# Kernel tuning notes

Measured on AMD Instinct MI355X. Metric: run time of the kernel, lower is better.

Reference implementation:

```python
import jax, jax.numpy as jnp
import numpy as np

N_NODES = 50000
N_EDGES = 800000
F_DIM = 128
K_RBF = 5
NUM_BLOCKS = 5
NUM_RES = 2  # residuals ModuleList is overwritten; only num_atom_residual layers exist
NUM_ELEM = 20
CUTOFF = 10.0
LOG2 = float(np.log(2.0))


def shifted_softplus(x):
    return jax.nn.softplus(x) - LOG2


def rbf_expand(D):
    # D: [E]; ExponentialRBF with cutoff=10, K=5.
    # softplus(softplus_inverse(x)) == x, so centers/widths are the raw values.
    centers = jnp.linspace(1.0, float(np.exp(-CUTOFF)), K_RBF)          # [K]
    width = jnp.float32((0.5 / ((1.0 - np.exp(-CUTOFF)) / K_RBF)) ** 2)  # scalar
    x = D / CUTOFF
    x3 = x ** 3; x4 = x3 * x; x5 = x4 * x
    cut = jnp.where(x < 1.0, 1.0 - 6.0 * x5 + 15.0 * x4 - 10.0 * x3, 0.0)  # [E]
    return cut[:, None] * jnp.exp(-width * (jnp.exp(-D)[:, None] - centers) ** 2)  # [E,K]


def residual(x, w1, b1, w2, b2):
    # ResidualLayer: x + dense2(dense1(act(x))) (dropout = identity in eval)
    y = shifted_softplus(x)
    return x + (y @ w1.T + b1) @ w2.T + b2


def setup_inputs() -> dict:
    key = jax.random.key(0)
    ks = jax.random.split(key, 20)
    s = 1.0 / np.sqrt(F_DIM)
    B, R = NUM_BLOCKS, NUM_RES
    inp = {
        'atom_types': jax.random.randint(ks[0], (N_NODES,), 0, NUM_ELEM),
        'edge_src': jax.random.randint(ks[1], (N_EDGES,), 0, N_NODES),
        'edge_dst': jax.random.randint(ks[2], (N_EDGES,), 0, N_NODES),
        'pos': jax.random.normal(ks[3], (N_NODES, 3), jnp.float32) * 3.0,
        'emb_table': jax.random.normal(ks[4], (NUM_ELEM, F_DIM), jnp.float32),
        'k2f_w': jax.random.normal(ks[5], (B, F_DIM, K_RBF), jnp.float32) * 0.4,
        'wi': jax.random.normal(ks[6], (B, F_DIM, F_DIM), jnp.float32) * s,
        'bi': jnp.zeros((B, F_DIM), jnp.float32),
        'wj': jax.random.normal(ks[7], (B, F_DIM, F_DIM), jnp.float32) * s,
        'bj': jnp.zeros((B, F_DIM), jnp.float32),
        'wd': jax.random.normal(ks[8], (B, F_DIM, F_DIM), jnp.float32) * s,
        'bd': jnp.zeros((B, F_DIM), jnp.float32),
        'u': jax.random.uniform(ks[9], (B, F_DIM), jnp.float32),
        'res_w1': jax.random.normal(ks[10], (B, R, F_DIM, F_DIM), jnp.float32) * s,
        'res_b1': jnp.zeros((B, R, F_DIM), jnp.float32),
        'res_w2': jax.random.normal(ks[11], (B, R, F_DIM, F_DIM), jnp.float32) * s,
        'res_b2': jnp.zeros((B, R, F_DIM), jnp.float32),
    }
    return inp


def reference(atom_types, edge_src, edge_dst, pos, emb_table,
              k2f_w, wi, bi, wj, bj, wd, bd, u,
              res_w1, res_b1, res_w2, res_b2):
    # edge distances and RBF features are geometry-only: compute once
    dist = jnp.linalg.norm(pos[edge_src] - pos[edge_dst], axis=-1)  # [E]
    rbf = rbf_expand(dist)                                          # [E,K]

    h = emb_table[atom_types]                                       # [N,F]
    for b in range(NUM_BLOCKS):
        x = shifted_softplus(h)  # pre-activation (dropout = identity)
        # dense_i / dense_j are linear -> apply on nodes, then gather per edge
        hi = x @ wi[b].T + bi[b]
        hj = x @ wj[b].T + bj[b]
        ai = hi[edge_dst]                                           # [E,F] target i
        g = rbf @ k2f_w[b].T                                        # [E,F]
        aj = g * hj[edge_src]                                       # [E,F]
        m = ai + aj
        for r in range(NUM_RES):
            m = residual(m, res_w1[b, r], res_b1[b, r], res_w2[b, r], res_b2[b, r])
        m = shifted_softplus(m)
        new = u[b] * ai + m @ wd[b].T + bd[b]
        for r in range(NUM_RES):  # same residual layers reused (as in source)
            new = residual(new, res_w1[b, r], res_b1[b, r], res_w2[b, r], res_b2[b, r])
        h = jax.ops.segment_sum(new, edge_dst, num_segments=N_NODES)  # aggr='add'
    return h
```

## Files before the change

### kernel.cpp

```cpp
#include <hip/hip_runtime.h>
#include <stdint.h>

#define FD 128
#define NNODES 50000
#define NEDGES 800000
#define EB 64

typedef __attribute__((ext_vector_type(8))) short v8s;
typedef __attribute__((ext_vector_type(4))) float v4f;

__device__ __forceinline__ unsigned short f2bf(float f) {
  union { float f; unsigned int u; } v; v.f = f;
  unsigned int r = v.u + 0x7fffu + ((v.u >> 16) & 1u);
  return (unsigned short)(r >> 16);
}
__device__ __forceinline__ float bf2f(unsigned short b) {
  union { unsigned int u; float f; } v; v.u = ((unsigned int)b) << 16;
  return v.f;
}
__device__ __forceinline__ float sspf(float x) {
  float e = __expf(-fabsf(x));
  return fmaxf(x, 0.0f) + __logf(1.0f + e) - 0.6931471805599453f;
}
__device__ __forceinline__ int swz(int row, int colel) {
  return row * FD + (colel ^ ((row & 7) << 3));
}

__device__ __forceinline__ void load_bfrag(const unsigned short* __restrict__ wfrag,
                                           int l, v8s (&Bf)[2][4]) {
#pragma unroll
  for (int ni = 0; ni < 2; ni++)
#pragma unroll
    for (int kk = 0; kk < 4; kk++)
      Bf[ni][kk] = *(const v8s*)(wfrag + (((ni << 2) + kk) << 9) + (l << 3));
}

template <int MI>
__device__ __forceinline__ void mfma_frag(const unsigned short* ACT, const v8s (&Bf)[2][4],
                                          int lc, int lg, v4f (&acc)[MI][2]) {
#pragma unroll
  for (int mi = 0; mi < MI; mi++) {
    v8s Af[4];
    int arow = mi * 16 + lc;
#pragma unroll
    for (int kk = 0; kk < 4; kk++)
      Af[kk] = *(const v8s*)&ACT[swz(arow, kk * 32 + lg * 8)];
#pragma unroll
    for (int ni = 0; ni < 2; ni++)
#pragma unroll
      for (int kk = 0; kk < 4; kk++)
        acc[mi][ni] = __builtin_amdgcn_mfma_f32_16x16x32_bf16(
            Af[kk], Bf[ni][kk], acc[mi][ni], 0, 0, 0);
  }
}


__global__ void rbf_kernel(const int* __restrict__ es, const int* __restrict__ ed,
                           const float* __restrict__ pos, float* __restrict__ rbf) {
  int e = blockIdx.x * 256 + threadIdx.x;
  if (e >= NEDGES) return;
  int s = es[e], d = ed[e];
  float dx = pos[s * 3 + 0] - pos[d * 3 + 0];
  float dy = pos[s * 3 + 1] - pos[d * 3 + 1];
  float dz = pos[s * 3 + 2] - pos[d * 3 + 2];
  float D = sqrtf(dx * dx + dy * dy + dz * dz);
  float x = D * 0.1f;
  float cut = 0.0f;
  if (x < 1.0f) {
    float x3 = x * x * x, x4 = x3 * x, x5 = x4 * x;
    cut = 1.0f - 6.0f * x5 + 15.0f * x4 - 10.0f * x3;
  }
  float eD = __expf(-D);
  float em10 = __expf(-10.0f);
  float wdt = 2.5f / (1.0f - em10);
  wdt = wdt * wdt;
#pragma unroll
  for (int k = 0; k < 5; k++) {
    float ck = 1.0f + (float)k * 0.25f * (em10 - 1.0f);
    float t = eD - ck;
    rbf[e * 5 + k] = cut * __expf(-wdt * t * t);
  }
}

__global__ void wconv_kernel(const float* __restrict__ wi, const float* __restrict__ wj,
                             const float* __restrict__ wd, const float* __restrict__ w1,
                             const float* __restrict__ w2, unsigned short* __restrict__ wimg2) {
  int i = blockIdx.x * 256 + threadIdx.x;
  if (i >= 5 * 7 * 16384) return;
  int b = i / (7 * 16384);
  int r = i - b * 7 * 16384;
  int mtx = r >> 14;
  int off = r & 16383;
  int j = off & 7;
  int l = (off >> 3) & 63;
  int kk = (off >> 9) & 3;
  int nt = off >> 11;
  int row = nt * 16 + (l & 15);
  int col = kk * 32 + (l >> 4) * 8 + j;
  const float* src;
  switch (mtx) {
    case 0: src = wi + (size_t)b * 16384; break;
    case 1: src = wj + (size_t)b * 16384; break;
    case 2: src = wd + (size_t)b * 16384; break;
    case 3: src = w1 + (size_t)(b * 2 + 0) * 16384; break;
    case 4: src = w2 + (size_t)(b * 2 + 0) * 16384; break;
    case 5: src = w1 + (size_t)(b * 2 + 1) * 16384; break;
    default: src = w2 + (size_t)(b * 2 + 1) * 16384; break;
  }
  wimg2[(size_t)(b * 7 + mtx) * 16384 + off] = f2bf(src[row * 128 + col]);
}

__global__ void h0_kernel(const int* __restrict__ at, const float* __restrict__ emb,
                          float* __restrict__ h) {
  int i = blockIdx.x * 256 + threadIdx.x;
  int n = i >> 7, c = i & 127;
  h[i] = emb[at[n] * FD + c];
}


__global__ __launch_bounds__(256, 3) void node_kernel(
    const float* __restrict__ h, const unsigned short* __restrict__ wblk,
    const float* __restrict__ bi, const float* __restrict__ bj,
    float* __restrict__ hi_f, unsigned short* __restrict__ hj_bf)
{
  __shared__ unsigned short ACT[FD * FD];
  const int tid = threadIdx.x;
  const int wv = tid >> 6;
  const int l = tid & 63;
  const int lc = l & 15;
  const int lg = l >> 4;
  const int col0 = wv * 32 + lc;
  const int rbase = lg * 4;
  const int n0 = blockIdx.x * 128;

  v8s Bfi[2][4], Bfj[2][4];
  load_bfrag(wblk + 0 * 16384 + wv * 4096, l, Bfi);
  load_bfrag(wblk + 1 * 16384 + wv * 4096, l, Bfj);

  float bvi[2], bvj[2];
#pragma unroll
  for (int ni = 0; ni < 2; ni++) {
    bvi[ni] = bi[col0 + ni * 16];
    bvj[ni] = bj[col0 + ni * 16];
  }

#pragma unroll
  for (int mi = 0; mi < 8; mi++) {
#pragma unroll
    for (int j = 0; j < 4; j++) {
      int row = mi * 16 + rbase + j;
      int n = n0 + row;
      int xorv = (row & 7) << 3;
#pragma unroll
      for (int ni = 0; ni < 2; ni++) {
        int c = col0 + ni * 16;
        float x = 0.0f;
        if (n < NNODES) x = sspf(h[n * FD + c]);
        ACT[row * FD + (c ^ xorv)] = f2bf(x);
      }
    }
  }
  __syncthreads();

  v4f acc[8][2];
#pragma unroll
  for (int mi = 0; mi < 8; mi++)
#pragma unroll
    for (int ni = 0; ni < 2; ni++)
      acc[mi][ni] = (v4f){bvi[ni], bvi[ni], bvi[ni], bvi[ni]};
  mfma_frag<8>(ACT, Bfi, lc, lg, acc);
#pragma unroll
  for (int mi = 0; mi < 8; mi++) {
#pragma unroll
    for (int j = 0; j < 4; j++) {
      int n = n0 + mi * 16 + rbase + j;
      if (n < NNODES) {
#pragma unroll
        for (int ni = 0; ni < 2; ni++)
          hi_f[n * FD + col0 + ni * 16] = acc[mi][ni][j];
      }
    }
  }

#pragma unroll
  for (int mi = 0; mi < 8; mi++)
#pragma unroll
    for (int ni = 0; ni < 2; ni++)
      acc[mi][ni] = (v4f){bvj[ni], bvj[ni], bvj[ni], bvj[ni]};
  mfma_frag<8>(ACT, Bfj, lc, lg, acc);
#pragma unroll
  for (int mi = 0; mi < 8; mi++) {
#pragma unroll
    for (int j = 0; j < 4; j++) {
      int n = n0 + mi * 16 + rbase + j;
      if (n < NNODES) {
#pragma unroll
        for (int ni = 0; ni < 2; ni++)
          hj_bf[n * FD + col0 + ni * 16] = f2bf(acc[mi][ni][j]);
      }
    }
  }
}


__global__ __launch_bounds__(256, 3) void edge_kernel(
    const float* __restrict__ hi_f, const unsigned short* __restrict__ hj_bf,
    const float* __restrict__ rbf, const int* __restrict__ esrc,
    const int* __restrict__ edst, const unsigned short* __restrict__ wblk,
    const float* __restrict__ rb1, const float* __restrict__ rb2,
    const float* __restrict__ bd, const float* __restrict__ uvec,
    const float* __restrict__ k2f, float* __restrict__ outp)
{
  __shared__ unsigned short ACTb[2][EB * FD];
  __shared__ float RBF5[EB * 5];
  __shared__ int EDG[2 * EB];

  const int tid = threadIdx.x;
  const int wv = tid >> 6;
  const int l = tid & 63;
  const int lc = l & 15;
  const int lg = l >> 4;
  const int col0 = wv * 32 + lc;
  const int rbase = lg * 4;
  const int e0 = blockIdx.x * EB;

  for (int i = tid; i < 2 * EB; i += 256) {
    EDG[i] = (i < EB) ? esrc[e0 + i] : edst[e0 + i - EB];
  }
  for (int i = tid; i < EB * 5; i += 256) RBF5[i] = rbf[e0 * 5 + i];

  float bt0[2], bt1[2], bt2[2], bt3[2], bt4[2], uu[2], kc[2][5];
#pragma unroll
  for (int ni = 0; ni < 2; ni++) {
    int c = col0 + ni * 16;
    bt0[ni] = rb1[c];
    bt1[ni] = rb2[c];
    bt2[ni] = rb1[FD + c];
    bt3[ni] = rb2[FD + c];
    bt4[ni] = bd[c];
    uu[ni] = uvec[c];
#pragma unroll
    for (int k = 0; k < 5; k++) kc[ni][k] = k2f[c * 5 + k];
  }
  __syncthreads();

  float m[4][2][4];
#pragma unroll
  for (int mi = 0; mi < 4; mi++) {
#pragma unroll
    for (int j = 0; j < 4; j++) {
      int row = mi * 16 + rbase + j;
      int s = EDG[row];
      int d = EDG[EB + row];
      int xorv = (row & 7) << 3;
      float r5[5];
#pragma unroll
      for (int k = 0; k < 5; k++) r5[k] = RBF5[row * 5 + k];
#pragma unroll
      for (int ni = 0; ni < 2; ni++) {
        int c = col0 + ni * 16;
        float ai = hi_f[d * FD + c];
        float hjv = bf2f(hj_bf[s * FD + c]);
        float g = r5[0] * kc[ni][0] + r5[1] * kc[ni][1] + r5[2] * kc[ni][2]
                + r5[3] * kc[ni][3] + r5[4] * kc[ni][4];
        float m0 = ai + g * hjv;
        m[mi][ni][j] = m0;
        ACTb[0][row * FD + (c ^ xorv)] = f2bf(sspf(m0));
      }
    }
  }

  int buf = 0;
#pragma unroll 1
  for (int L = 0; L < 9; L++) {
    int mat = (L == 4) ? 2 : ((L < 4) ? 3 + L : L - 2);
    v8s Bf[2][4];
    load_bfrag(wblk + mat * 16384 + wv * 4096, l, Bf);

    v4f acc[4][2];
    if (L == 4) {
#pragma unroll
      for (int mi = 0; mi < 4; mi++) {
#pragma unroll
        for (int j = 0; j < 4; j++) {
          int d = EDG[EB + mi * 16 + rbase + j];
#pragma unroll
          for (int ni = 0; ni < 2; ni++)
            acc[mi][ni][j] = uu[ni] * hi_f[d * FD + col0 + ni * 16] + bt4[ni];
        }
      }
    } else {
      int Lr = (L < 4) ? L : L - 5;
      float bv[2];
#pragma unroll
      for (int ni = 0; ni < 2; ni++)
        bv[ni] = (Lr == 0) ? bt0[ni] : (Lr == 1) ? bt1[ni] : (Lr == 2) ? bt2[ni] : bt3[ni];
#pragma unroll
      for (int mi = 0; mi < 4; mi++)
#pragma unroll
        for (int ni = 0; ni < 2; ni++)
          acc[mi][ni] = (v4f){bv[ni], bv[ni], bv[ni], bv[ni]};
    }

    __syncthreads();
    mfma_frag<4>(&ACTb[buf][0], Bf, lc, lg, acc);

    const bool isAcc = (L == 1) || (L == 3) || (L == 6) || (L == 8);
    if (L == 4) {
#pragma unroll
      for (int mi = 0; mi < 4; mi++)
#pragma unroll
        for (int ni = 0; ni < 2; ni++)
#pragma unroll
          for (int j = 0; j < 4; j++) m[mi][ni][j] = acc[mi][ni][j];
    } else if (isAcc) {
#pragma unroll
      for (int mi = 0; mi < 4; mi++)
#pragma unroll
        for (int ni = 0; ni < 2; ni++)
#pragma unroll
          for (int j = 0; j < 4; j++) m[mi][ni][j] += acc[mi][ni][j];
    }

    if (L < 8) {
      const bool wssp = isAcc || (L == 4);
      unsigned short* An = &ACTb[buf ^ 1][0];
#pragma unroll
      for (int mi = 0; mi < 4; mi++) {
#pragma unroll
        for (int j = 0; j < 4; j++) {
          int row = mi * 16 + rbase + j;
          int xorv = (row & 7) << 3;
#pragma unroll
          for (int ni = 0; ni < 2; ni++) {
            int c = col0 + ni * 16;
            float v = wssp ? sspf(m[mi][ni][j]) : acc[mi][ni][j];
            An[row * FD + (c ^ xorv)] = f2bf(v);
          }
        }
      }
    }
    buf ^= 1;
  }

#pragma unroll
  for (int mi = 0; mi < 4; mi++) {
#pragma unroll
    for (int j = 0; j < 4; j++) {
      int d = EDG[EB + mi * 16 + rbase + j];
#pragma unroll
      for (int ni = 0; ni < 2; ni++)
        atomicAdd(&outp[d * FD + col0 + ni * 16], m[mi][ni][j]);
    }
  }
}

extern "C" void kernel_launch(void* const* d_in, const int* in_sizes, int n_in,
                              void* d_out, int out_size, void* d_ws, size_t ws_size,
                              hipStream_t stream) {
  (void)in_sizes; (void)n_in; (void)out_size; (void)ws_size;
  const int* at = (const int*)d_in[0];
  const int* es = (const int*)d_in[1];
  const int* ed = (const int*)d_in[2];
  const float* pos = (const float*)d_in[3];
  const float* emb = (const float*)d_in[4];
  const float* k2f = (const float*)d_in[5];
  const float* wi = (const float*)d_in[6];
  const float* bi = (const float*)d_in[7];
  const float* wj = (const float*)d_in[8];
  const float* bj = (const float*)d_in[9];
  const float* wd = (const float*)d_in[10];
  const float* bd = (const float*)d_in[11];
  const float* u = (const float*)d_in[12];
  const float* rw1 = (const float*)d_in[13];
  const float* rb1 = (const float*)d_in[14];
  const float* rw2 = (const float*)d_in[15];
  const float* rb2 = (const float*)d_in[16];

  char* w = (char*)d_ws;
  float* rbf = (float*)w;                     w += (size_t)NEDGES * 5 * 4;
  float* hi_f = (float*)w;                    w += (size_t)NNODES * FD * 4;
  unsigned short* hj_bf = (unsigned short*)w; w += (size_t)NNODES * FD * 2;
  float* hA = (float*)w;                      w += (size_t)NNODES * FD * 4;
  unsigned short* wimg2 = (unsigned short*)w; w += (size_t)5 * 7 * 16384 * 2;

  rbf_kernel<<<(NEDGES + 255) / 256, 256, 0, stream>>>(es, ed, pos, rbf);
  wconv_kernel<<<(5 * 7 * 16384 + 255) / 256, 256, 0, stream>>>(wi, wj, wd, rw1, rw2, wimg2);
  h0_kernel<<<(NNODES * FD) / 256, 256, 0, stream>>>(at, emb, hA);

  float* hcur = hA;
  for (int b = 0; b < 5; b++) {
    node_kernel<<<(NNODES + 127) / 128, 256, 0, stream>>>(
        hcur, wimg2 + (size_t)b * 7 * 16384, bi + b * FD, bj + b * FD, hi_f, hj_bf);
    float* tgt = (b & 1) ? hA : (float*)d_out;
    hipMemsetAsync(tgt, 0, (size_t)NNODES * FD * 4, stream);
    edge_kernel<<<NEDGES / EB, 256, 0, stream>>>(
        hi_f, hj_bf, rbf, es, ed, wimg2 + (size_t)b * 7 * 16384,
        rb1 + (size_t)b * 2 * FD, rb2 + (size_t)b * 2 * FD, bd + b * FD,
        u + b * FD, k2f + (size_t)b * FD * 5, tgt);
    hcur = tgt;
  }
}
```

Baseline: 5.512 ms.

## Swap MFMA operand order so each lane owns contiguous feature columns

The MFMA operands are swapped so the weight fragment is the A operand and activations are the B operand. Each lane's accumulator now holds four consecutive feature columns of one node or edge, instead of four rows of one column. This allows vectorized 16-byte float loads and stores, 8-byte packed bf16 LDS writes, and vectorized gathers of hi/hj per edge, replacing scalar strided accesses. Edge-kernel biases move to shared memory and launch bounds rise to 4 blocks per CU, which adds register pressure and changes the atomic scatter pattern.

```diff
diff --git a/kernel.cpp b/kernel.cpp
--- a/kernel.cpp
+++ b/kernel.cpp
@@ -22,36 +22,20 @@
   float e = __expf(-fabsf(x));
   return fmaxf(x, 0.0f) + __logf(1.0f + e) - 0.6931471805599453f;
 }
-__device__ __forceinline__ int swz(int row, int colel) {
-  return row * FD + (colel ^ ((row & 7) << 3));
+__device__ __forceinline__ uint2 pack4(float a, float b, float c, float d) {
+  uint2 r;
+  r.x = (unsigned)f2bf(a) | ((unsigned)f2bf(b) << 16);
+  r.y = (unsigned)f2bf(c) | ((unsigned)f2bf(d) << 16);
+  return r;
 }
 
 __device__ __forceinline__ void load_bfrag(const unsigned short* __restrict__ wfrag,
-                                           int l, v8s (&Bf)[2][4]) {
+                                           int l, v8s (&Wf)[2][4]) {
 #pragma unroll
   for (int ni = 0; ni < 2; ni++)
 #pragma unroll
     for (int kk = 0; kk < 4; kk++)
-      Bf[ni][kk] = *(const v8s*)(wfrag + (((ni << 2) + kk) << 9) + (l << 3));
-}
-
-template <int MI>
-__device__ __forceinline__ void mfma_frag(const unsigned short* ACT, const v8s (&Bf)[2][4],
-                                          int lc, int lg, v4f (&acc)[MI][2]) {
-#pragma unroll
-  for (int mi = 0; mi < MI; mi++) {
-    v8s Af[4];
-    int arow = mi * 16 + lc;
-#pragma unroll
-    for (int kk = 0; kk < 4; kk++)
-      Af[kk] = *(const v8s*)&ACT[swz(arow, kk * 32 + lg * 8)];
-#pragma unroll
-    for (int ni = 0; ni < 2; ni++)
-#pragma unroll
-      for (int kk = 0; kk < 4; kk++)
-        acc[mi][ni] = __builtin_amdgcn_mfma_f32_16x16x32_bf16(
-            Af[kk], Bf[ni][kk], acc[mi][ni], 0, 0, 0);
-  }
+      Wf[ni][kk] = *(const v8s*)(wfrag + (((ni << 2) + kk) << 9) + (l << 3));
 }
 
 
@@ -118,92 +102,78 @@
 }
 
 
-__global__ __launch_bounds__(256, 3) void node_kernel(
+__global__ __launch_bounds__(256, 4) void node_kernel(
     const float* __restrict__ h, const unsigned short* __restrict__ wblk,
     const float* __restrict__ bi, const float* __restrict__ bj,
     float* __restrict__ hi_f, unsigned short* __restrict__ hj_bf)
 {
-  __shared__ unsigned short ACT[FD * FD];
+  __shared__ __align__(16) unsigned short ACT[FD * FD];
   const int tid = threadIdx.x;
   const int wv = tid >> 6;
   const int l = tid & 63;
   const int lc = l & 15;
   const int lg = l >> 4;
-  const int col0 = wv * 32 + lc;
-  const int rbase = lg * 4;
+  const int cq = wv * 32 + lg * 4;
   const int n0 = blockIdx.x * 128;
 
-  v8s Bfi[2][4], Bfj[2][4];
-  load_bfrag(wblk + 0 * 16384 + wv * 4096, l, Bfi);
-  load_bfrag(wblk + 1 * 16384 + wv * 4096, l, Bfj);
-
-  float bvi[2], bvj[2];
+  {
+    int row = tid >> 1;
+    int ch = (tid & 1) * 64;
+    int n = n0 + row;
+    int x8 = (row & 7) << 3;
+#pragma unroll
+    for (int q = 0; q < 16; q++) {
+      int ce = ch + q * 4;
+      v4f hv = (v4f){0.f, 0.f, 0.f, 0.f};
+      if (n < NNODES) hv = *(const v4f*)&h[(size_t)n * FD + ce];
+      uint2 p = pack4(sspf(hv[0]), sspf(hv[1]), sspf(hv[2]), sspf(hv[3]));
+      *(uint2*)&ACT[row * FD + (ce ^ x8)] = p;
+    }
+  }
+
+  v8s Wfi[2][4], Wfj[2][4];
+  load_bfrag(wblk + 0 * 16384 + wv * 4096, l, Wfi);
+  load_bfrag(wblk + 1 * 16384 + wv * 4096, l, Wfj);
+  v4f biq[2], bjq[2];
 #pragma unroll
   for (int ni = 0; ni < 2; ni++) {
-    bvi[ni] = bi[col0 + ni * 16];
-    bvj[ni] = bj[col0 + ni * 16];
-  }
-
-#pragma unroll
-  for (int mi = 0; mi < 8; mi++) {
-#pragma unroll
-    for (int j = 0; j < 4; j++) {
-      int row = mi * 16 + rbase + j;
-      int n = n0 + row;
-      int xorv = (row & 7) << 3;
+    biq[ni] = *(const v4f*)&bi[cq + ni * 16];
+    bjq[ni] = *(const v4f*)&bj[cq + ni * 16];
+  }
+  __syncthreads();
+
+  const int x8 = (lc & 7) << 3;
+#pragma unroll 1
+  for (int ti = 0; ti < 8; ti++) {
+    int node = ti * 16 + lc;
+    v8s Af[4];
+#pragma unroll
+    for (int kk = 0; kk < 4; kk++)
+      Af[kk] = *(const v8s*)&ACT[node * FD + ((kk * 32 + lg * 8) ^ x8)];
+    v4f ai[2], aj[2];
+#pragma unroll
+    for (int ni = 0; ni < 2; ni++) { ai[ni] = biq[ni]; aj[ni] = bjq[ni]; }
+#pragma unroll
+    for (int ni = 0; ni < 2; ni++)
+#pragma unroll
+      for (int kk = 0; kk < 4; kk++) {
+        ai[ni] = __builtin_amdgcn_mfma_f32_16x16x32_bf16(Wfi[ni][kk], Af[kk], ai[ni], 0, 0, 0);
+        aj[ni] = __builtin_amdgcn_mfma_f32_16x16x32_bf16(Wfj[ni][kk], Af[kk], aj[ni], 0, 0, 0);
+      }
+    int n = n0 + node;
+    if (n < NNODES) {
 #pragma unroll
       for (int ni = 0; ni < 2; ni++) {
-        int c = col0 + ni * 16;
-        float x = 0.0f;
-        if (n < NNODES) x = sspf(h[n * FD + c]);
-        ACT[row * FD + (c ^ xorv)] = f2bf(x);
-      }
-    }
-  }
-  __syncthreads();
-
-  v4f acc[8][2];
-#pragma unroll
-  for (int mi = 0; mi < 8; mi++)
-#pragma unroll
-    for (int ni = 0; ni < 2; ni++)
-      acc[mi][ni] = (v4f){bvi[ni], bvi[ni], bvi[ni], bvi[ni]};
-  mfma_frag<8>(ACT, Bfi, lc, lg, acc);
-#pragma unroll
-  for (int mi = 0; mi < 8; mi++) {
-#pragma unroll
-    for (int j = 0; j < 4; j++) {
-      int n = n0 + mi * 16 + rbase + j;
-      if (n < NNODES) {
-#pragma unroll
-        for (int ni = 0; ni < 2; ni++)
-          hi_f[n * FD + col0 + ni * 16] = acc[mi][ni][j];
-      }
-    }
-  }
-
-#pragma unroll
-  for (int mi = 0; mi < 8; mi++)
-#pragma unroll
-    for (int ni = 0; ni < 2; ni++)
-      acc[mi][ni] = (v4f){bvj[ni], bvj[ni], bvj[ni], bvj[ni]};
-  mfma_frag<8>(ACT, Bfj, lc, lg, acc);
-#pragma unroll
-  for (int mi = 0; mi < 8; mi++) {
-#pragma unroll
-    for (int j = 0; j < 4; j++) {
-      int n = n0 + mi * 16 + rbase + j;
-      if (n < NNODES) {
-#pragma unroll
-        for (int ni = 0; ni < 2; ni++)
-          hj_bf[n * FD + col0 + ni * 16] = f2bf(acc[mi][ni][j]);
-      }
-    }
-  }
-}
-
-
-__global__ __launch_bounds__(256, 3) void edge_kernel(
+        *(v4f*)&hi_f[(size_t)n * FD + cq + ni * 16] = ai[ni];
+        *(uint2*)&hj_bf[(size_t)n * FD + cq + ni * 16] =
+            pack4(aj[ni][0], aj[ni][1], aj[ni][2], aj[ni][3]);
+      }
+    }
+  }
+}
+
+
+__global__ __launch_bounds__(256, 4) void edge_kernel(
     const float* __restrict__ hi_f, const unsigned short* __restrict__ hj_bf,
     const float* __restrict__ rbf, const int* __restrict__ esrc,
     const int* __restrict__ edst, const unsigned short* __restrict__ wblk,
@@ -211,7 +181,8 @@
     const float* __restrict__ bd, const float* __restrict__ uvec,
     const float* __restrict__ k2f, float* __restrict__ outp)
 {
-  __shared__ unsigned short ACTb[2][EB * FD];
+  __shared__ __align__(16) unsigned short ACTb[2][EB * FD];
+  __shared__ float BIAS[6 * FD];
   __shared__ float RBF5[EB * 5];
   __shared__ int EDG[2 * EB];
 
@@ -220,53 +191,66 @@
   const int l = tid & 63;
   const int lc = l & 15;
   const int lg = l >> 4;
-  const int col0 = wv * 32 + lc;
-  const int rbase = lg * 4;
+  const int cq = wv * 32 + lg * 4;
+  const int x8 = (lc & 7) << 3;
   const int e0 = blockIdx.x * EB;
 
-  for (int i = tid; i < 2 * EB; i += 256) {
+  for (int i = tid; i < 2 * EB; i += 256)
     EDG[i] = (i < EB) ? esrc[e0 + i] : edst[e0 + i - EB];
-  }
   for (int i = tid; i < EB * 5; i += 256) RBF5[i] = rbf[e0 * 5 + i];
-
-  float bt0[2], bt1[2], bt2[2], bt3[2], bt4[2], uu[2], kc[2][5];
-#pragma unroll
-  for (int ni = 0; ni < 2; ni++) {
-    int c = col0 + ni * 16;
-    bt0[ni] = rb1[c];
-    bt1[ni] = rb2[c];
-    bt2[ni] = rb1[FD + c];
-    bt3[ni] = rb2[FD + c];
-    bt4[ni] = bd[c];
-    uu[ni] = uvec[c];
-#pragma unroll
-    for (int k = 0; k < 5; k++) kc[ni][k] = k2f[c * 5 + k];
-  }
+  for (int i = tid; i < 6 * FD; i += 256) {
+    int which = i >> 7, c = i & 127;
+    float v;
+    switch (which) {
+      case 0: v = rb1[c]; break;
+      case 1: v = rb2[c]; break;
+      case 2: v = rb1[FD + c]; break;
+      case 3: v = rb2[FD + c]; break;
+      case 4: v = bd[c]; break;
+      default: v = uvec[c]; break;
+    }
+    BIAS[i] = v;
+  }
+
+  v4f kcq[2][5];
+#pragma unroll
+  for (int ni = 0; ni < 2; ni++)
+#pragma unroll
+    for (int w = 0; w < 5; w++)
+      kcq[ni][w] = *(const v4f*)&k2f[(cq + ni * 16) * 5 + w * 4];
+
   __syncthreads();
 
-  float m[4][2][4];
-#pragma unroll
-  for (int mi = 0; mi < 4; mi++) {
-#pragma unroll
-    for (int j = 0; j < 4; j++) {
-      int row = mi * 16 + rbase + j;
-      int s = EDG[row];
-      int d = EDG[EB + row];
-      int xorv = (row & 7) << 3;
-      float r5[5];
-#pragma unroll
-      for (int k = 0; k < 5; k++) r5[k] = RBF5[row * 5 + k];
-#pragma unroll
-      for (int ni = 0; ni < 2; ni++) {
-        int c = col0 + ni * 16;
-        float ai = hi_f[d * FD + c];
-        float hjv = bf2f(hj_bf[s * FD + c]);
-        float g = r5[0] * kc[ni][0] + r5[1] * kc[ni][1] + r5[2] * kc[ni][2]
-                + r5[3] * kc[ni][3] + r5[4] * kc[ni][4];
-        float m0 = ai + g * hjv;
-        m[mi][ni][j] = m0;
-        ACTb[0][row * FD + (c ^ xorv)] = f2bf(sspf(m0));
-      }
+  int dN[4];
+  v4f m[2][4];
+#pragma unroll
+  for (int ei = 0; ei < 4; ei++) {
+    int row = ei * 16 + lc;
+    int s = EDG[row];
+    int d = EDG[EB + row];
+    dN[ei] = d;
+    float r5[5];
+#pragma unroll
+    for (int k = 0; k < 5; k++) r5[k] = RBF5[row * 5 + k];
+#pragma unroll
+    for (int ni = 0; ni < 2; ni++) {
+      int c = cq + ni * 16;
+      v4f ai = *(const v4f*)&hi_f[(size_t)d * FD + c];
+      uint2 hp = *(const uint2*)&hj_bf[(size_t)s * FD + c];
+      float hjf[4] = {bf2f((unsigned short)(hp.x & 0xffff)), bf2f((unsigned short)(hp.x >> 16)),
+                      bf2f((unsigned short)(hp.y & 0xffff)), bf2f((unsigned short)(hp.y >> 16))};
+#pragma unroll
+      for (int r = 0; r < 4; r++) {
+        float g = 0.f;
+#pragma unroll
+        for (int k = 0; k < 5; k++) {
+          int fi = r * 5 + k;
+          g += r5[k] * kcq[ni][fi >> 2][fi & 3];
+        }
+        m[ni][ei][r] = ai[r] + g * hjf[r];
+      }
+      *(uint2*)&ACTb[0][row * FD + (c ^ x8)] =
+          pack4(sspf(m[ni][ei][0]), sspf(m[ni][ei][1]), sspf(m[ni][ei][2]), sspf(m[ni][ei][3]));
     }
   }
 
@@ -274,69 +258,84 @@
 #pragma unroll 1
   for (int L = 0; L < 9; L++) {
     int mat = (L == 4) ? 2 : ((L < 4) ? 3 + L : L - 2);
-    v8s Bf[2][4];
-    load_bfrag(wblk + mat * 16384 + wv * 4096, l, Bf);
-
-    v4f acc[4][2];
+    v8s Wf[2][4];
+    load_bfrag(wblk + mat * 16384 + wv * 4096, l, Wf);
+
+    v4f acc[2][4];
     if (L == 4) {
-#pragma unroll
-      for (int mi = 0; mi < 4; mi++) {
-#pragma unroll
-        for (int j = 0; j < 4; j++) {
-          int d = EDG[EB + mi * 16 + rbase + j];
-#pragma unroll
-          for (int ni = 0; ni < 2; ni++)
-            acc[mi][ni][j] = uu[ni] * hi_f[d * FD + col0 + ni * 16] + bt4[ni];
+      v4f uq[2], bq[2];
+#pragma unroll
+      for (int ni = 0; ni < 2; ni++) {
+        uq[ni] = *(const v4f*)&BIAS[5 * FD + cq + ni * 16];
+        bq[ni] = *(const v4f*)&BIAS[4 * FD + cq + ni * 16];
+      }
+#pragma unroll
+      for (int ei = 0; ei < 4; ei++) {
+        int d = dN[ei];
+#pragma unroll
+        for (int ni = 0; ni < 2; ni++) {
+          v4f ai = *(const v4f*)&hi_f[(size_t)d * FD + cq + ni * 16];
+#pragma unroll
+          for (int r = 0; r < 4; r++) acc[ni][ei][r] = uq[ni][r] * ai[r] + bq[ni][r];
         }
       }
     } else {
-      int Lr = (L < 4) ? L : L - 5;
-      float bv[2];
+      int bidx = (L < 4) ? L : L - 5;
+      v4f bq[2];
+#pragma unroll
+      for (int ni = 0; ni < 2; ni++) bq[ni] = *(const v4f*)&BIAS[bidx * FD + cq + ni * 16];
+#pragma unroll
+      for (int ei = 0; ei < 4; ei++)
+#pragma unroll
+        for (int ni = 0; ni < 2; ni++) acc[ni][ei] = bq[ni];
+    }
+
+    __syncthreads();
+
+    const unsigned short* A = &ACTb[buf][0];
+#pragma unroll
+    for (int ei = 0; ei < 4; ei++) {
+      int rb = (ei * 16 + lc) * FD;
+      v8s Af[4];
+#pragma unroll
+      for (int kk = 0; kk < 4; kk++)
+        Af[kk] = *(const v8s*)&A[rb + ((kk * 32 + lg * 8) ^ x8)];
 #pragma unroll
       for (int ni = 0; ni < 2; ni++)
-        bv[ni] = (Lr == 0) ? bt0[ni] : (Lr == 1) ? bt1[ni] : (Lr == 2) ? bt2[ni] : bt3[ni];
-#pragma unroll
-      for (int mi = 0; mi < 4; mi++)
-#pragma unroll
-        for (int ni = 0; ni < 2; ni++)
-          acc[mi][ni] = (v4f){bv[ni], bv[ni], bv[ni], bv[ni]};
-    }
-
-    __syncthreads();
-    mfma_frag<4>(&ACTb[buf][0], Bf, lc, lg, acc);
+#pragma unroll
+        for (int kk = 0; kk < 4; kk++)
+          acc[ni][ei] = __builtin_amdgcn_mfma_f32_16x16x32_bf16(Wf[ni][kk], Af[kk],
+                                                               acc[ni][ei], 0, 0, 0);
+    }
 
     const bool isAcc = (L == 1) || (L == 3) || (L == 6) || (L == 8);
     if (L == 4) {
 #pragma unroll
-      for (int mi = 0; mi < 4; mi++)
-#pragma unroll
-        for (int ni = 0; ni < 2; ni++)
-#pragma unroll
-          for (int j = 0; j < 4; j++) m[mi][ni][j] = acc[mi][ni][j];
+      for (int ei = 0; ei < 4; ei++)
+#pragma unroll
+        for (int ni = 0; ni < 2; ni++) m[ni][ei] = acc[ni][ei];
     } else if (isAcc) {
 #pragma unroll
-      for (int mi = 0; mi < 4; mi++)
-#pragma unroll
-        for (int ni = 0; ni < 2; ni++)
-#pragma unroll
-          for (int j = 0; j < 4; j++) m[mi][ni][j] += acc[mi][ni][j];
+      for (int ei = 0; ei < 4; ei++)
+#pragma unroll
+        for (int ni = 0; ni < 2; ni++) m[ni][ei] += acc[ni][ei];
     }
 
     if (L < 8) {
       const bool wssp = isAcc || (L == 4);
       unsigned short* An = &ACTb[buf ^ 1][0];
 #pragma unroll
-      for (int mi = 0; mi < 4; mi++) {
-#pragma unroll
-        for (int j = 0; j < 4; j++) {
-          int row = mi * 16 + rbase + j;
-          int xorv = (row & 7) << 3;
-#pragma unroll
-          for (int ni = 0; ni < 2; ni++) {
-            int c = col0 + ni * 16;
-            float v = wssp ? sspf(m[mi][ni][j]) : acc[mi][ni][j];
-            An[row * FD + (c ^ xorv)] = f2bf(v);
-          }
+      for (int ei = 0; ei < 4; ei++) {
+        int rb = (ei * 16 + lc) * FD;
+#pragma unroll
+        for (int ni = 0; ni < 2; ni++) {
+          uint2 p;
+          if (wssp)
+            p = pack4(sspf(m[ni][ei][0]), sspf(m[ni][ei][1]),
+                      sspf(m[ni][ei][2]), sspf(m[ni][ei][3]));
+          else
+            p = pack4(acc[ni][ei][0], acc[ni][ei][1], acc[ni][ei][2], acc[ni][ei][3]);
+          *(uint2*)&An[rb + ((cq + ni * 16) ^ x8)] = p;
         }
       }
     }
@@ -344,14 +343,13 @@
   }
 
 #pragma unroll
-  for (int mi = 0; mi < 4; mi++) {
-#pragma unroll
-    for (int j = 0; j < 4; j++) {
-      int d = EDG[EB + mi * 16 + rbase + j];
-#pragma unroll
-      for (int ni = 0; ni < 2; ni++)
-        atomicAdd(&outp[d * FD + col0 + ni * 16], m[mi][ni][j]);
-    }
+  for (int ei = 0; ei < 4; ei++) {
+    int d = dN[ei];
+#pragma unroll
+    for (int ni = 0; ni < 2; ni++)
+#pragma unroll
+      for (int r = 0; r < 4; r++)
+        atomicAdd(&outp[(size_t)d * FD + cq + ni * 16 + r], m[ni][ei][r]);
   }
 }
 
```

Measured after the change: 7.432 ms. 34.8% more time.
